# Kernel tuning notes

Measured on AMD Instinct MI355X. Metric: run time of the kernel, lower is better.

The kernel has to match this reference:

```python
import jax, jax.numpy as jnp
import numpy as np

B, C, H, W = 64, 3, 512, 512
P = 16
D = P * P          # 256 = patch_size**2 (token dim)
GH, GW = H // P, W // P
NP = GH * GW       # 1024 patches
HID = 1024         # FFN hidden
L = 6              # num_layers
NC = 1000          # num_classes
EPS = 1e-5


def setup_inputs() -> dict:
    key = jax.random.key(0)
    ks = jax.random.split(key, 8)
    n = lambda i, shape, scale=0.02: jax.random.normal(ks[i], shape, jnp.float32) * scale
    return dict(
        x=jax.random.normal(ks[0], (B, C, H, W), jnp.float32),
        conv_w=n(1, (D, C, P, P)),
        conv_b=jnp.zeros((D,), jnp.float32),
        pos_emb=n(2, (1, NP + 1, D), 1.0),
        cls_tok=n(3, (1, 1, D), 1.0),
        ln1_s=jnp.ones((L, D), jnp.float32), ln1_b=jnp.zeros((L, D), jnp.float32),
        ln2_s=jnp.ones((L, D), jnp.float32), ln2_b=jnp.zeros((L, D), jnp.float32),
        w1=n(4, (L, D, HID)), b1=jnp.zeros((L, HID), jnp.float32),
        w2=n(5, (L, HID, D)), b2=jnp.zeros((L, D), jnp.float32),
        head_ln_s=jnp.ones((D,), jnp.float32), head_ln_b=jnp.zeros((D,), jnp.float32),
        head_w=n(6, (D, NC)), head_b=jnp.zeros((NC,), jnp.float32),
    )


def _ln(x, s, b):
    m = x.mean(-1, keepdims=True)
    v = ((x - m) ** 2).mean(-1, keepdims=True)
    return (x - m) * jax.lax.rsqrt(v + EPS) * s + b


def reference(x, conv_w, conv_b, pos_emb, cls_tok,
              ln1_s, ln1_b, ln2_s, ln2_b, w1, b1, w2, b2,
              head_ln_s, head_ln_b, head_w, head_b):
    b = x.shape[0]
    # patch-embed conv (kernel==stride) as reshape + einsum
    xr = x.reshape(b, C, GH, P, GW, P)
    tok = jnp.einsum('bchpwq,dcpq->bhwd', xr, conv_w).reshape(b, NP, D) + conv_b
    t = jnp.concatenate([jnp.broadcast_to(cls_tok, (b, 1, D)), tok], axis=1) + pos_emb
    for i in range(L):
        # FNet token mixing: real part of 2D FFT over (tokens, dim)
        h = _ln(t, ln1_s[i], ln1_b[i])
        t = t + jnp.fft.fft2(h, axes=(-2, -1)).real
        # FFN
        h = _ln(t, ln2_s[i], ln2_b[i])
        h = jax.nn.leaky_relu(h @ w1[i] + b1[i], negative_slope=0.01) @ w2[i] + b2[i]
        t = t + h
    pooled = t.mean(axis=1)
    logits = _ln(pooled, head_ln_s, head_ln_b) @ head_w + head_b
    return jax.nn.softmax(logits, axis=-1)
```

## Files before the change

### kernel.cpp

```cpp
#include <hip/hip_runtime.h>
#include <math.h>

#define BATCH 64
#define CIN 3
#define IMH 512
#define IMW 512
#define PSZ 16
#define DIM 256
#define GHN 32
#define GWN 32
#define NTOK 1025
#define HID 1024
#define NLAYER 6
#define NCLS 1000
#define LN_EPS 1e-5f

#define KF 576
#define KR 640
#define MF 144
#define MROWS 65600

typedef __attribute__((ext_vector_type(8))) short short8;
typedef __attribute__((ext_vector_type(4))) float f32x4;

#define MFMA16(acc, a, b) acc = __builtin_amdgcn_mfma_f32_16x16x32_bf16(a, b, acc, 0, 0, 0)

__device__ inline unsigned short rne_bf16(float x) {
    unsigned u = __float_as_uint(x);
    return (unsigned short)((u + 0x7FFF + ((u >> 16) & 1)) >> 16);
}
__device__ inline void split_bf16(float x, unsigned short& hi, unsigned short& lo) {
    unsigned short h = rne_bf16(x);
    hi = h;
    float hf = __uint_as_float((unsigned)h << 16);
    lo = rne_bf16(x - hf);
}
__device__ inline float wave_sum(float v) {
#pragma unroll
    for (int off = 32; off; off >>= 1) v += __shfl_xor(v, off);
    return v;
}
__device__ inline short8 ld8x64(const unsigned short* lds, int row, int q) {
    return *(const short8*)(lds + (row * 8 + (q ^ (row & 7))) * 8);
}
__device__ inline short8 ld8x32(const unsigned short* lds, int row, int q) {
    return *(const short8*)(lds + (row * 4 + (q ^ ((row >> 1) & 3))) * 8);
}
__device__ inline void gl2lds16(const unsigned short* g, unsigned short* l) {
    __builtin_amdgcn_global_load_lds((const __attribute__((address_space(1))) unsigned int*)g,
                                     (__attribute__((address_space(3))) unsigned int*)l, 16, 0, 0);
}
__device__ inline void a_stage128(unsigned short* lds, const unsigned short* g, int lda, int tid, int maxrow) {
    int lane = tid & 63, w = tid >> 6;
#pragma unroll
    for (int s = 0; s < 4; s++) {
        int slot = w * 256 + s * 64;
        int sl = slot + lane;
        int row = sl >> 3, gc = (sl & 7) ^ (row & 7);
        if (row > maxrow) row = maxrow;
        gl2lds16(g + (size_t)row * lda + gc * 8, lds + slot * 8);
    }
}
__device__ inline void a_stage128_512(unsigned short* lds, const unsigned short* g, int lda, int tid, int maxrow) {
    int lane = tid & 63, w = tid >> 6;
#pragma unroll
    for (int s = 0; s < 2; s++) {
        int slot = w * 128 + s * 64;
        int sl = slot + lane;
        int row = sl >> 3, gc = (sl & 7) ^ (row & 7);
        if (row > maxrow) row = maxrow;
        gl2lds16(g + (size_t)row * lda + gc * 8, lds + slot * 8);
    }
}
__device__ inline void b_stage128x32(unsigned short* lds, const unsigned short* g, int lda, int tid) {
    int lane = tid & 63;
#pragma unroll
    for (int s = 0; s < 2; s++) {
        int slot = s * 256 + (tid >> 6) * 64;
        int sl = slot + lane;
        int row = sl >> 2, gc = (sl & 3) ^ ((row >> 1) & 3);
        gl2lds16(g + (size_t)row * lda + gc * 8, lds + slot * 8);
    }
}
__device__ inline void a_stage144x32(unsigned short* lds, const unsigned short* g, int lda, int tid) {
    int lane = tid & 63, w = tid >> 6;
#pragma unroll
    for (int s = 0; s < 2; s++) {
        int slot = s * 256 + w * 64;
        int sl = slot + lane;
        int row = sl >> 2, gc = (sl & 3) ^ ((row >> 1) & 3);
        gl2lds16(g + (size_t)row * lda + gc * 8, lds + slot * 8);
    }
    if (w == 0) {
        int slot = 512;
        int sl = slot + lane;
        int row = sl >> 2, gc = (sl & 3) ^ ((row >> 1) & 3);
        gl2lds16(g + (size_t)row * lda + gc * 8, lds + slot * 8);
    }
}

__global__ __launch_bounds__(256) void gen_dft2(unsigned short* C1h, unsigned short* C1l,
                                                unsigned short* S1h, unsigned short* S1l,
                                                unsigned short* C2h, unsigned short* C2l,
                                                unsigned short* S2h, unsigned short* S2l) {
    int idx = blockIdx.x * 256 + threadIdx.x;
    if (idx < KR * KF) {
        int k = idx / KF, n = idx - k * KF;
        float c = 0.f, s = 0.f;
        if (k <= 512 && n <= 512) {
            int r = (k * n) % 1025;
            double ang = 6.283185307179586476925287 * (double)r / 1025.0;
            c = (float)cos(ang); s = (float)sin(ang);
        }
        unsigned short h, l;
        split_bf16(c, h, l); C1h[idx] = h; C1l[idx] = l;
        split_bf16(s, h, l); S1h[idx] = h; S1l[idx] = l;
    }
    if (idx < 256 * 256) {
        int k = idx >> 8, n = idx & 255;
        int r = (k * n) & 255;
        double ang = 6.283185307179586476925287 * (double)r / 256.0;
        float c = (float)cos(ang), s = (float)sin(ang);
        unsigned short h, l;
        split_bf16(c, h, l); C2h[idx] = h; C2l[idx] = l;
        split_bf16(s, h, l); S2h[idx] = h; S2l[idx] = l;
    }
}

__global__ __launch_bounds__(256) void conv_wp(const float* __restrict__ w,
                                               unsigned short* __restrict__ wph, unsigned short* __restrict__ wpl) {
    int idx = blockIdx.x * 256 + threadIdx.x;
    unsigned short h, l;
    split_bf16(w[idx], h, l);
    wph[idx] = h; wpl[idx] = l;
}
__global__ __launch_bounds__(256) void conv_w1t(const float* __restrict__ w1, unsigned short* __restrict__ w1t) {
    int idx = blockIdx.x * 256 + threadIdx.x;
    int l = idx / 262144, rem = idx - l * 262144;
    int n = rem >> 8, k = rem & 255;
    w1t[idx] = rne_bf16(w1[(size_t)l * 262144 + (size_t)k * 1024 + n]);
}
__global__ __launch_bounds__(256) void conv_w2t(const float* __restrict__ w2, unsigned short* __restrict__ w2t) {
    int idx = blockIdx.x * 256 + threadIdx.x;
    int l = idx / 262144, rem = idx - l * 262144;
    int n = rem >> 10, k = rem & 1023;
    w2t[idx] = rne_bf16(w2[(size_t)l * 262144 + (size_t)k * 256 + n]);
}

__global__ __launch_bounds__(256) void cls_init(const float* __restrict__ cls, const float* __restrict__ pos,
                                                float* __restrict__ t) {
    int b = blockIdx.x, tid = threadIdx.x;
    t[(size_t)b * NTOK * DIM + tid] = cls[tid] + pos[tid];
}

__global__ __launch_bounds__(256) void patch_fused(const float* __restrict__ x,
                                                   const unsigned short* __restrict__ wph,
                                                   const unsigned short* __restrict__ wpl,
                                                   const float* __restrict__ cb, const float* __restrict__ pos,
                                                   float* __restrict__ t) {
    __shared__ __align__(16) unsigned short sAh[4096], sAl[4096], sBh[4096], sBl[4096];
    int m0 = blockIdx.x * 128, n0 = blockIdx.y * 128;
    int tid = threadIdx.x, lane = tid & 63, w = tid >> 6;
    int wr = (w >> 1) * 64, wc = (w & 1) * 64;
    f32x4 z = {0.f, 0.f, 0.f, 0.f};
    f32x4 acc[4][4] = {{z, z, z, z}, {z, z, z, z}, {z, z, z, z}, {z, z, z, z}};
    for (int k0 = 0; k0 < 768; k0 += 32) {
#pragma unroll
        for (int s = 0; s < 4; s++) {
            int lin = s * 1024 + tid * 4;
            int row = lin >> 5, kc = lin & 31;
            int m = m0 + row;
            int bb = m >> 10, gh = (m >> 5) & 31, gw = m & 31;
            int k = k0 + kc;
            int c = k >> 8, pp = (k >> 4) & 15, q = k & 15;
            const float* gp = x + (size_t)bb * 786432 + c * 262144 + gh * 8192 + pp * 512 + gw * 16 + q;
            float4 v = *(const float4*)gp;
            ushort4 oh, ol;
            split_bf16(v.x, oh.x, ol.x); split_bf16(v.y, oh.y, ol.y);
            split_bf16(v.z, oh.z, ol.z); split_bf16(v.w, oh.w, ol.w);
            int g = kc >> 3, half = (kc >> 2) & 1;
            int addr = (row * 4 + (g ^ ((row >> 1) & 3))) * 8 + half * 4;
            *(ushort4*)(sAh + addr) = oh;
            *(ushort4*)(sAl + addr) = ol;
        }
        b_stage128x32(sBh, wph + (size_t)n0 * 768 + k0, 768, tid);
        b_stage128x32(sBl, wpl + (size_t)n0 * 768 + k0, 768, tid);
        __syncthreads();
        int q = lane >> 4;
        short8 ah[4], al[4], bh8[4], bl8[4];
#pragma unroll
        for (int i = 0; i < 4; i++) {
            ah[i] = ld8x32(sAh, wr + i * 16 + (lane & 15), q);
            al[i] = ld8x32(sAl, wr + i * 16 + (lane & 15), q);
            bh8[i] = ld8x32(sBh, wc + i * 16 + (lane & 15), q);
            bl8[i] = ld8x32(sBl, wc + i * 16 + (lane & 15), q);
        }
#pragma unroll
        for (int i = 0; i < 4; i++)
#pragma unroll
            for (int j = 0; j < 4; j++) {
                MFMA16(acc[i][j], ah[i], bh8[j]);
                MFMA16(acc[i][j], ah[i], bl8[j]);
                MFMA16(acc[i][j], al[i], bh8[j]);
            }
        __syncthreads();
    }
    int q4 = (lane >> 4) * 4;
#pragma unroll
    for (int i = 0; i < 4; i++) {
        int r = m0 + wr + i * 16 + q4;
#pragma unroll
        for (int j = 0; j < 4; j++) {
            int c = n0 + wc + j * 16 + (lane & 15);
#pragma unroll
            for (int g = 0; g < 4; g++) {
                int rr = r + g;
                int bb = rr >> 10, tok = 1 + (rr & 1023);
                t[((size_t)bb * NTOK + tok) * 256 + c] =
                    acc[i][j][g] + cb[c] + pos[(size_t)tok * 256 + c];
            }
        }
    }
}

__global__ __launch_bounds__(256) void ln_stats(const float* __restrict__ t, float2* __restrict__ stats) {
    int wave = threadIdx.x >> 6, lane = threadIdx.x & 63;
    int m = blockIdx.x * 4 + wave;
    const float* row = t + (size_t)m * DIM;
    float4 v = *(const float4*)(row + lane * 4);
    float mean = wave_sum(v.x + v.y + v.z + v.w) * (1.f / 256.f);
    float dx = v.x - mean, dy = v.y - mean, dz = v.z - mean, dw = v.w - mean;
    float sq = wave_sum(dx * dx + dy * dy + dz * dz + dw * dw);
    float rstd = rsqrtf(sq * (1.f / 256.f) + LN_EPS);
    if (lane == 0) stats[m] = make_float2(mean, rstd);
}

__global__ __launch_bounds__(256) void ln2_bf16(const float* __restrict__ t, unsigned short* __restrict__ hh,
                                                const float* __restrict__ s, const float* __restrict__ bb) {
    int wave = threadIdx.x >> 6, lane = threadIdx.x & 63;
    int m = blockIdx.x * 4 + wave;
    const float* row = t + (size_t)m * DIM;
    float4 v = *(const float4*)(row + lane * 4);
    float mean = wave_sum(v.x + v.y + v.z + v.w) * (1.f / 256.f);
    float dx = v.x - mean, dy = v.y - mean, dz = v.z - mean, dw = v.w - mean;
    float sq = wave_sum(dx * dx + dy * dy + dz * dz + dw * dw);
    float rstd = rsqrtf(sq * (1.f / 256.f) + LN_EPS);
    float4 s4 = *(const float4*)(s + lane * 4);
    float4 b4 = *(const float4*)(bb + lane * 4);
    ushort4 o;
    o.x = rne_bf16(dx * rstd * s4.x + b4.x);
    o.y = rne_bf16(dy * rstd * s4.y + b4.y);
    o.z = rne_bf16(dz * rstd * s4.z + b4.z);
    o.w = rne_bf16(dw * rstd * s4.w + b4.w);
    *(ushort4*)(hh + (size_t)m * DIM + lane * 4) = o;
}

__global__ __launch_bounds__(256) void fold_gemm(
    const float* __restrict__ tt, const float2* __restrict__ stats,
    const float* __restrict__ ls, const float* __restrict__ lb,
    const unsigned short* __restrict__ C2h, const unsigned short* __restrict__ C2l,
    const unsigned short* __restrict__ S2h, const unsigned short* __restrict__ S2l,
    unsigned short* __restrict__ Ycth, unsigned short* __restrict__ Yctl,
    unsigned short* __restrict__ Ysth, unsigned short* __restrict__ Ystl) {
    __shared__ __align__(16) unsigned short sAh[4096], sAl[4096], sBh[4608], sBl[4608];
    int m0 = blockIdx.x * 128;
    int zz = blockIdx.y;
    const unsigned short* Bh = zz ? S2h : C2h;
    const unsigned short* Bl = zz ? S2l : C2l;
    unsigned short* Oh = zz ? Ysth : Ycth;
    unsigned short* Ol = zz ? Ystl : Yctl;
    int tid = threadIdx.x, lane = tid & 63, w = tid >> 6;
    int wr = w * 32;
    f32x4 zf = {0.f, 0.f, 0.f, 0.f};
    f32x4 acc[2][9];
#pragma unroll
    for (int i = 0; i < 2; i++)
#pragma unroll
        for (int j = 0; j < 9; j++) acc[i][j] = zf;
    for (int k0 = 0; k0 < 256; k0 += 32) {
#pragma unroll
        for (int s = 0; s < 4; s++) {
            int sl = tid + s * 256;
            int row = sl >> 3, g = sl & 7;
            int r = m0 + row;
            int b = r / KF, np = r - b * KF;
            float4 hv = {0.f, 0.f, 0.f, 0.f};
            if (np <= 512) {
                int d0 = k0 + g * 4;
                float4 s4 = *(const float4*)(ls + d0);
                float4 b4 = *(const float4*)(lb + d0);
                int i1 = b * NTOK + np;
                float2 st1 = stats[i1];
                float4 va = *(const float4*)(tt + (size_t)i1 * 256 + d0);
                float hax = (va.x - st1.x) * st1.y * s4.x + b4.x;
                float hay = (va.y - st1.x) * st1.y * s4.y + b4.y;
                float haz = (va.z - st1.x) * st1.y * s4.z + b4.z;
                float haw = (va.w - st1.x) * st1.y * s4.w + b4.w;
                float hbx = 0.f, hby = 0.f, hbz = 0.f, hbw = 0.f;
                if (np >= 1) {
                    int i2 = b * NTOK + (NTOK - np);
                    float2 st2 = stats[i2];
                    float4 vb = *(const float4*)(tt + (size_t)i2 * 256 + d0);
                    hbx = (vb.x - st2.x) * st2.y * s4.x + b4.x;
                    hby = (vb.y - st2.x) * st2.y * s4.y + b4.y;
                    hbz = (vb.z - st2.x) * st2.y * s4.z + b4.z;
                    hbw = (vb.w - st2.x) * st2.y * s4.w + b4.w;
                }
                if (zz) { hv.x = hax - hbx; hv.y = hay - hby; hv.z = haz - hbz; hv.w = haw - hbw; }
                else    { hv.x = hax + hbx; hv.y = hay + hby; hv.z = haz + hbz; hv.w = haw + hbw; }
            }
            ushort4 oh, ol;
            split_bf16(hv.x, oh.x, ol.x); split_bf16(hv.y, oh.y, ol.y);
            split_bf16(hv.z, oh.z, ol.z); split_bf16(hv.w, oh.w, ol.w);
            int addr = (row * 4 + ((g >> 1) ^ ((row >> 1) & 3))) * 8 + (g & 1) * 4;
            *(ushort4*)(sAh + addr) = oh;
            *(ushort4*)(sAl + addr) = ol;
        }
        a_stage144x32(sBh, Bh + k0, 256, tid);
        a_stage144x32(sBl, Bl + k0, 256, tid);
        __syncthreads();
        int q = lane >> 4;
        short8 ah[2], al[2];
#pragma unroll
        for (int i = 0; i < 2; i++) {
            int r = wr + i * 16 + (lane & 15);
            ah[i] = ld8x32(sAh, r, q); al[i] = ld8x32(sAl, r, q);
        }
#pragma unroll
        for (int j = 0; j < 9; j++) {
            int rb = j * 16 + (lane & 15);
            short8 bh = ld8x32(sBh, rb, q), bl = ld8x32(sBl, rb, q);
#pragma unroll
            for (int i = 0; i < 2; i++) {
                MFMA16(acc[i][j], ah[i], bh);
                MFMA16(acc[i][j], ah[i], bl);
                MFMA16(acc[i][j], al[i], bh);
            }
        }
        __syncthreads();
    }
    int q4 = (lane >> 4) * 4;
#pragma unroll
    for (int i = 0; i < 2; i++) {
        int r = m0 + wr + i * 16 + q4;
        int bidx = r / KF, kp = r - bidx * KF;
#pragma unroll
        for (int j = 0; j < 9; j++) {
            int c = j * 16 + (lane & 15);
            ushort4 oh, ol;
            split_bf16(acc[i][j][0], oh.x, ol.x);
            split_bf16(acc[i][j][1], oh.y, ol.y);
            split_bf16(acc[i][j][2], oh.z, ol.z);
            split_bf16(acc[i][j][3], oh.w, ol.w);
            size_t off = ((size_t)bidx * MF + c) * KF + kp;
            *(ushort4*)(Oh + off) = oh;
            *(ushort4*)(Ol + off) = ol;
        }
    }
}

__global__ __launch_bounds__(512, 6) void fft_big_dual(
    const unsigned short* __restrict__ C1h, const unsigned short* __restrict__ C1l,
    const unsigned short* __restrict__ S1h, const unsigned short* __restrict__ S1l,
    const unsigned short* __restrict__ Ych, const unsigned short* __restrict__ Ycl,
    const unsigned short* __restrict__ Ysh, const unsigned short* __restrict__ Ysl,
    float* __restrict__ t) {
    __shared__ __align__(16) unsigned short sC1h[4096], sC1l[4096], sS1h[4096], sS1l[4096];
    __shared__ __align__(16) unsigned short sYch[2048], sYcl[2048], sYsh[2048], sYsl[2048];
    int k0m = blockIdx.x * 128, n0 = blockIdx.y * 64;
    int tid = threadIdx.x, lane = tid & 63, w = tid >> 6;
    int wr = (w >> 1) * 32, wc = (w & 1) * 32;
    f32x4 z = {0.f, 0.f, 0.f, 0.f};
    f32x4 U[2][2], V[2][2];
#pragma unroll
    for (int i = 0; i < 2; i++)
#pragma unroll
        for (int j = 0; j < 2; j++) { U[i][j] = z; V[i][j] = z; }
    for (int kk0 = 0; kk0 < KF; kk0 += 32) {
        {
            int row = tid >> 2, gc = (tid & 3) ^ ((row >> 1) & 3);
            size_t ga = (size_t)k0m * KF + kk0 + (size_t)row * KF + gc * 8;
            unsigned short* lbase0 = sC1h + (size_t)(w * 64) * 8;
            unsigned short* lbase1 = sC1l + (size_t)(w * 64) * 8;
            unsigned short* lbase2 = sS1h + (size_t)(w * 64) * 8;
            unsigned short* lbase3 = sS1l + (size_t)(w * 64) * 8;
            gl2lds16(C1h + ga, lbase0);
            gl2lds16(C1l + ga, lbase1);
            gl2lds16(S1h + ga, lbase2);
            gl2lds16(S1l + ga, lbase3);
        }
        {
            int m = w >> 1, p = w & 1;
            const unsigned short* yg;
            unsigned short* yl;
            if (m == 0)      { yg = Ych; yl = sYch; }
            else if (m == 1) { yg = Ycl; yl = sYcl; }
            else if (m == 2) { yg = Ysh; yl = sYsh; }
            else             { yg = Ysl; yl = sYsl; }
            size_t gb = (size_t)n0 * KF + kk0;
#pragma unroll
            for (int s = 0; s < 2; s++) {
                int slot = p * 128 + s * 64;
                int sl = slot + lane;
                int row = sl >> 2, gc = (sl & 3) ^ ((row >> 1) & 3);
                gl2lds16(yg + gb + (size_t)row * KF + gc * 8, yl + slot * 8);
            }
        }
        __syncthreads();
        int q = lane >> 4;
        short8 bch[2], bcl[2], bsh[2], bsl[2];
#pragma unroll
        for (int j = 0; j < 2; j++) {
            int r2 = wc + j * 16 + (lane & 15);
            bch[j] = ld8x32(sYch, r2, q); bcl[j] = ld8x32(sYcl, r2, q);
            bsh[j] = ld8x32(sYsh, r2, q); bsl[j] = ld8x32(sYsl, r2, q);
        }
#pragma unroll
        for (int i = 0; i < 2; i++) {
            int r1 = wr + i * 16 + (lane & 15);
            short8 ach = ld8x32(sC1h, r1, q), acl = ld8x32(sC1l, r1, q);
            short8 ash = ld8x32(sS1h, r1, q), asl = ld8x32(sS1l, r1, q);
#pragma unroll
            for (int j = 0; j < 2; j++) {
                MFMA16(U[i][j], ach, bch[j]);
                MFMA16(U[i][j], ach, bcl[j]);
                MFMA16(U[i][j], acl, bch[j]);
                MFMA16(V[i][j], ash, bsh[j]);
                MFMA16(V[i][j], ash, bsl[j]);
                MFMA16(V[i][j], asl, bsh[j]);
            }
        }
        __syncthreads();
    }
    int q4 = (lane >> 4) * 4;
#pragma unroll
    for (int j = 0; j < 2; j++) {
        int rcol = n0 + wc + j * 16 + (lane & 15);
        int b = rcol / MF, mm = rcol - b * MF;
        float* tb = t + (size_t)b * NTOK * DIM;
        if (mm > 128) continue;
#pragma unroll
        for (int i = 0; i < 2; i++) {
            int kk = k0m + wr + i * 16 + q4;
#pragma unroll
            for (int g = 0; g < 4; g++) {
                int k = kk + g;
                if (k > 512) continue;
                float u = U[i][j][g], v = V[i][j][g];
                tb[(size_t)k * 256 + mm] += u - v;
                if (mm >= 1 && mm <= 127) tb[(size_t)k * 256 + 256 - mm] += u + v;
                if (k >= 1) {
                    tb[(size_t)(NTOK - k) * 256 + mm] += u + v;
                    if (mm >= 1 && mm <= 127) tb[(size_t)(NTOK - k) * 256 + 256 - mm] += u - v;
                }
            }
        }
    }
}

__global__ __launch_bounds__(512) void gemm_ffn_fused(
    const unsigned short* __restrict__ A, const unsigned short* __restrict__ W1t,
    const float* __restrict__ b1, const unsigned short* __restrict__ W2t,
    const float* __restrict__ b2, float* __restrict__ t) {
    __shared__ __align__(16) unsigned short sB[32768];
    __shared__ __align__(16) unsigned short sH[16384];
    int m0 = blockIdx.x * 128;
    int tid = threadIdx.x, lane = tid & 63, w = tid >> 6;
    int wr1 = (w >> 1) * 32, wc1 = (w & 1) * 64;
    int wr2 = (w >> 2) * 64, wc2 = (w & 3) * 64;
    short8 areg[2][8];
#pragma unroll
    for (int i = 0; i < 2; i++) {
        int rr = m0 + wr1 + i * 16 + (lane & 15);
        if (rr > MROWS - 1) rr = MROWS - 1;
        const unsigned short* ap = A + (size_t)rr * 256 + (lane >> 4) * 8;
#pragma unroll
        for (int p = 0; p < 4; p++)
#pragma unroll
            for (int kc = 0; kc < 2; kc++)
                areg[i][p * 2 + kc] = *(const short8*)(ap + p * 64 + kc * 32);
    }
    f32x4 z = {0.f, 0.f, 0.f, 0.f};
    f32x4 acc2[4][4] = {{z, z, z, z}, {z, z, z, z}, {z, z, z, z}, {z, z, z, z}};
    int q4 = (lane >> 4) * 4;
    for (int hc = 0; hc < 8; hc++) {
        int h0 = hc * 128;
        __syncthreads();
#pragma unroll
        for (int p = 0; p < 4; p++)
            a_stage128_512(sB + p * 8192, W1t + (size_t)h0 * 256 + p * 64, 256, tid, 127);
        __syncthreads();
        f32x4 acc1[2][4] = {{z, z, z, z}, {z, z, z, z}};
#pragma unroll
        for (int p = 0; p < 4; p++)
#pragma unroll
            for (int kc = 0; kc < 2; kc++) {
                int q = (lane >> 4) + kc * 4;
                short8 bh[4];
#pragma unroll
                for (int j = 0; j < 4; j++)
                    bh[j] = ld8x64(sB + p * 8192, wc1 + j * 16 + (lane & 15), q);
#pragma unroll
                for (int i = 0; i < 2; i++)
#pragma unroll
                    for (int j = 0; j < 4; j++) MFMA16(acc1[i][j], areg[i][p * 2 + kc], bh[j]);
            }
#pragma unroll
        for (int j = 0; j < 4; j++) {
            int col = wc1 + j * 16 + (lane & 15);
            float bv = b1[h0 + col];
            int panel = col >> 6, c64 = col & 63;
#pragma unroll
            for (int i = 0; i < 2; i++)
#pragma unroll
                for (int g = 0; g < 4; g++) {
                    int row = wr1 + i * 16 + q4 + g;
                    float val = acc1[i][j][g] + bv;
                    val = val > 0.f ? val : 0.01f * val;
                    sH[panel * 8192 + (row * 8 + ((c64 >> 3) ^ (row & 7))) * 8 + (c64 & 7)] = rne_bf16(val);
                }
        }
        __syncthreads();
#pragma unroll
        for (int hp = 0; hp < 2; hp++)
#pragma unroll
            for (int rb = 0; rb < 2; rb++)
                a_stage128_512(sB + hp * 16384 + rb * 8192,
                               W2t + (size_t)(rb * 128) * 1024 + h0 + hp * 64, 1024, tid, 127);
        __syncthreads();
#pragma unroll
        for (int hp = 0; hp < 2; hp++)
#pragma unroll
            for (int kc = 0; kc < 2; kc++) {
                int q = (lane >> 4) + kc * 4;
                short8 ah[4], bh[4];
#pragma unroll
                for (int i = 0; i < 4; i++)
                    ah[i] = ld8x64(sH + hp * 8192, wr2 + i * 16 + (lane & 15), q);
#pragma unroll
                for (int j = 0; j < 4; j++)
                    bh[j] = ld8x64(sB + hp * 16384, wc2 + j * 16 + (lane & 15), q);
#pragma unroll
                for (int i = 0; i < 4; i++)
#pragma unroll
                    for (int j = 0; j < 4; j++) MFMA16(acc2[i][j], ah[i], bh[j]);
            }
    }
#pragma unroll
    for (int i = 0; i < 4; i++) {
        int r = m0 + wr2 + i * 16 + q4;
#pragma unroll
        for (int j = 0; j < 4; j++) {
            int c = wc2 + j * 16 + (lane & 15);
            float bv = b2[c];
#pragma unroll
            for (int g = 0; g < 4; g++) {
                int rr = r + g;
                if (rr < MROWS) t[(size_t)rr * 256 + c] += acc2[i][j][g] + bv;
            }
        }
    }
}

__global__ __launch_bounds__(256) void head_kernel(const float* __restrict__ t,
                                                   const float* __restrict__ hs, const float* __restrict__ hb,
                                                   const float* __restrict__ hw, const float* __restrict__ hbias,
                                                   float* __restrict__ out) {
    __shared__ float red[256];
    __shared__ float lnv[256];
    int b = blockIdx.x, tid = threadIdx.x;
    const float* tb = t + (size_t)b * NTOK * DIM;
    float s = 0.f;
    for (int m = 0; m < NTOK; m++) s += tb[m * DIM + tid];
    s *= (1.f / 1025.f);
    red[tid] = s;
    __syncthreads();
    for (int off = 128; off; off >>= 1) {
        if (tid < off) red[tid] += red[tid + off];
        __syncthreads();
    }
    float mean = red[0] * (1.f / 256.f);
    __syncthreads();
    float d = s - mean;
    red[tid] = d * d;
    __syncthreads();
    for (int off = 128; off; off >>= 1) {
        if (tid < off) red[tid] += red[tid + off];
        __syncthreads();
    }
    float rstd = rsqrtf(red[0] * (1.f / 256.f) + LN_EPS);
    __syncthreads();
    lnv[tid] = d * rstd * hs[tid] + hb[tid];
    __syncthreads();
    float lo[4];
#pragma unroll
    for (int jj = 0; jj < 4; jj++) {
        int n = tid + jj * 256;
        float a = -1e30f;
        if (n < NCLS) {
            a = hbias[n];
            for (int dd = 0; dd < DIM; dd++) a += lnv[dd] * hw[dd * NCLS + n];
        }
        lo[jj] = a;
    }
    float mx = fmaxf(fmaxf(lo[0], lo[1]), fmaxf(lo[2], lo[3]));
    red[tid] = mx;
    __syncthreads();
    for (int off = 128; off; off >>= 1) {
        if (tid < off) red[tid] = fmaxf(red[tid], red[tid + off]);
        __syncthreads();
    }
    float gmax = red[0];
    __syncthreads();
    float ev[4];
    float es = 0.f;
#pragma unroll
    for (int jj = 0; jj < 4; jj++) {
        int n = tid + jj * 256;
        ev[jj] = 0.f;
        if (n < NCLS) {
            ev[jj] = expf(lo[jj] - gmax);
            es += ev[jj];
        }
    }
    red[tid] = es;
    __syncthreads();
    for (int off = 128; off; off >>= 1) {
        if (tid < off) red[tid] += red[tid + off];
        __syncthreads();
    }
    float inv = 1.f / red[0];
#pragma unroll
    for (int jj = 0; jj < 4; jj++) {
        int n = tid + jj * 256;
        if (n < NCLS) out[(size_t)b * NCLS + n] = ev[jj] * inv;
    }
}

extern "C" void kernel_launch(void* const* d_in, const int* in_sizes, int n_in,
                              void* d_out, int out_size, void* d_ws, size_t ws_size,
                              hipStream_t stream) {
    const float* x      = (const float*)d_in[0];
    const float* conv_w = (const float*)d_in[1];
    const float* conv_b = (const float*)d_in[2];
    const float* pos    = (const float*)d_in[3];
    const float* cls    = (const float*)d_in[4];
    const float* ln1_s  = (const float*)d_in[5];
    const float* ln1_b  = (const float*)d_in[6];
    const float* ln2_s  = (const float*)d_in[7];
    const float* ln2_b  = (const float*)d_in[8];
    const float* w1     = (const float*)d_in[9];
    const float* b1     = (const float*)d_in[10];
    const float* w2     = (const float*)d_in[11];
    const float* b2     = (const float*)d_in[12];
    const float* hls    = (const float*)d_in[13];
    const float* hlb    = (const float*)d_in[14];
    const float* hw     = (const float*)d_in[15];
    const float* hbias  = (const float*)d_in[16];
    float* out = (float*)d_out;
    char* W = (char*)d_ws;

    float*          t    = (float*)(W + 0ULL);
    char*           pool = W + 67174400ULL;
    unsigned short* Ycth = (unsigned short*)(pool + 75497472ULL);
    unsigned short* Yctl = (unsigned short*)(pool + 75497472ULL + 10616832ULL);
    unsigned short* Ysth = (unsigned short*)(pool + 75497472ULL + 2 * 10616832ULL);
    unsigned short* Ystl = (unsigned short*)(pool + 75497472ULL + 3 * 10616832ULL);
    unsigned short* hh   = (unsigned short*)(pool + 134348800ULL);
    unsigned short* C1h  = (unsigned short*)(W + 235110400ULL);
    unsigned short* C1l  = (unsigned short*)(W + 235110400ULL + 737280ULL);
    unsigned short* S1h  = (unsigned short*)(W + 235110400ULL + 2 * 737280ULL);
    unsigned short* S1l  = (unsigned short*)(W + 235110400ULL + 3 * 737280ULL);
    unsigned short* C2h  = (unsigned short*)(W + 238059520ULL);
    unsigned short* C2l  = (unsigned short*)(W + 238059520ULL + 131072ULL);
    unsigned short* S2h  = (unsigned short*)(W + 238059520ULL + 2 * 131072ULL);
    unsigned short* S2l  = (unsigned short*)(W + 238059520ULL + 3 * 131072ULL);
    unsigned short* w1t  = (unsigned short*)(W + 238583808ULL);
    unsigned short* w2t  = (unsigned short*)(W + 241729536ULL);
    unsigned short* wph  = (unsigned short*)(W + 244875264ULL);
    unsigned short* wpl  = (unsigned short*)(W + 245268480ULL);
    float2*         stats = (float2*)(W + 245661696ULL);

    gen_dft2<<<dim3(1440), dim3(256), 0, stream>>>(C1h, C1l, S1h, S1l, C2h, C2l, S2h, S2l);
    conv_wp<<<dim3(768), dim3(256), 0, stream>>>(conv_w, wph, wpl);
    conv_w1t<<<dim3(6144), dim3(256), 0, stream>>>(w1, w1t);
    conv_w2t<<<dim3(6144), dim3(256), 0, stream>>>(w2, w2t);
    cls_init<<<dim3(BATCH), dim3(256), 0, stream>>>(cls, pos, t);
    patch_fused<<<dim3(512, 2), dim3(256), 0, stream>>>(x, wph, wpl, conv_b, pos, t);

    for (int l = 0; l < NLAYER; l++) {
        ln_stats<<<dim3(16400), dim3(256), 0, stream>>>(t, stats);
        fold_gemm<<<dim3(288, 2), dim3(256), 0, stream>>>(
            t, stats, ln1_s + l * DIM, ln1_b + l * DIM,
            C2h, C2l, S2h, S2l, Ycth, Yctl, Ysth, Ystl);
        fft_big_dual<<<dim3(5, 144), dim3(512), 0, stream>>>(
            C1h, C1l, S1h, S1l, Ycth, Yctl, Ysth, Ystl, t);
        ln2_bf16<<<dim3(16400), dim3(256), 0, stream>>>(t, hh, ln2_s + l * DIM, ln2_b + l * DIM);
        gemm_ffn_fused<<<dim3(513), dim3(512), 0, stream>>>(
            hh, w1t + (size_t)l * 262144, b1 + (size_t)l * HID,
            w2t + (size_t)l * 262144, b2 + (size_t)l * DIM, t);
    }
    head_kernel<<<dim3(BATCH), dim3(256), 0, stream>>>(t, hls, hlb, hw, hbias, out);
}
```

Before: 2.735 ms.

## Shrink FFN hidden chunk to 64 and prefetch next W1 chunk during GEMM2

The fused FFN kernel now walks the hidden dimension in 16 chunks of 64 instead of 8 chunks of 128. LDS use drops from 96KB to 80KB, split into separate W1/W2/H buffers, and launch bounds ask for more resident blocks. The next W1 chunk is loaded asynchronously into LDS while the second GEMM runs on the current chunk, removing a barrier-separated staging phase per iteration. The cost is twice as many loop iterations and barriers, plus smaller MFMA work per sync.

Result: slower. 4.024 ms (+47.1%).

```diff
diff --git a/kernel.cpp b/kernel.cpp
--- a/kernel.cpp
+++ b/kernel.cpp
@@ -458,16 +458,18 @@
     }
 }
 
-__global__ __launch_bounds__(512) void gemm_ffn_fused(
+__global__ __launch_bounds__(512, 4) void gemm_ffn_fused(
     const unsigned short* __restrict__ A, const unsigned short* __restrict__ W1t,
     const float* __restrict__ b1, const unsigned short* __restrict__ W2t,
     const float* __restrict__ b2, float* __restrict__ t) {
-    __shared__ __align__(16) unsigned short sB[32768];
-    __shared__ __align__(16) unsigned short sH[16384];
+    __shared__ __align__(16) unsigned short sW1[16384];
+    __shared__ __align__(16) unsigned short sW2[16384];
+    __shared__ __align__(16) unsigned short sH[8192];
     int m0 = blockIdx.x * 128;
     int tid = threadIdx.x, lane = tid & 63, w = tid >> 6;
-    int wr1 = (w >> 1) * 32, wc1 = (w & 1) * 64;
+    int wr1 = (w >> 1) * 32, wc1 = (w & 1) * 32;
     int wr2 = (w >> 2) * 64, wc2 = (w & 3) * 64;
+    int prow = tid >> 3, pgc = (tid & 7) ^ (prow & 7);
     short8 areg[2][8];
 #pragma unroll
     for (int i = 0; i < 2; i++) {
@@ -483,33 +485,34 @@
     f32x4 z = {0.f, 0.f, 0.f, 0.f};
     f32x4 acc2[4][4] = {{z, z, z, z}, {z, z, z, z}, {z, z, z, z}, {z, z, z, z}};
     int q4 = (lane >> 4) * 4;
-    for (int hc = 0; hc < 8; hc++) {
-        int h0 = hc * 128;
-        __syncthreads();
-#pragma unroll
-        for (int p = 0; p < 4; p++)
-            a_stage128_512(sB + p * 8192, W1t + (size_t)h0 * 256 + p * 64, 256, tid, 127);
-        __syncthreads();
-        f32x4 acc1[2][4] = {{z, z, z, z}, {z, z, z, z}};
+#pragma unroll
+    for (int p = 0; p < 4; p++)
+        gl2lds16(W1t + (size_t)prow * 256 + p * 64 + pgc * 8, sW1 + p * 4096 + (w * 64) * 8);
+    for (int hc = 0; hc < 16; hc++) {
+        int h0 = hc * 64;
+#pragma unroll
+        for (int rb = 0; rb < 2; rb++)
+            a_stage128_512(sW2 + rb * 8192, W2t + (size_t)(rb * 128) * 1024 + h0, 1024, tid, 127);
+        __syncthreads();
+        f32x4 acc1[2][2] = {{z, z}, {z, z}};
 #pragma unroll
         for (int p = 0; p < 4; p++)
 #pragma unroll
             for (int kc = 0; kc < 2; kc++) {
                 int q = (lane >> 4) + kc * 4;
-                short8 bh[4];
-#pragma unroll
-                for (int j = 0; j < 4; j++)
-                    bh[j] = ld8x64(sB + p * 8192, wc1 + j * 16 + (lane & 15), q);
+                short8 bh[2];
+#pragma unroll
+                for (int j = 0; j < 2; j++)
+                    bh[j] = ld8x64(sW1 + p * 4096, wc1 + j * 16 + (lane & 15), q);
 #pragma unroll
                 for (int i = 0; i < 2; i++)
 #pragma unroll
-                    for (int j = 0; j < 4; j++) MFMA16(acc1[i][j], areg[i][p * 2 + kc], bh[j]);
-            }
-#pragma unroll
-        for (int j = 0; j < 4; j++) {
+                    for (int j = 0; j < 2; j++) MFMA16(acc1[i][j], areg[i][p * 2 + kc], bh[j]);
+            }
+#pragma unroll
+        for (int j = 0; j < 2; j++) {
             int col = wc1 + j * 16 + (lane & 15);
             float bv = b1[h0 + col];
-            int panel = col >> 6, c64 = col & 63;
 #pragma unroll
             for (int i = 0; i < 2; i++)
 #pragma unroll
@@ -517,34 +520,34 @@
                     int row = wr1 + i * 16 + q4 + g;
                     float val = acc1[i][j][g] + bv;
                     val = val > 0.f ? val : 0.01f * val;
-                    sH[panel * 8192 + (row * 8 + ((c64 >> 3) ^ (row & 7))) * 8 + (c64 & 7)] = rne_bf16(val);
+                    sH[(row * 8 + ((col >> 3) ^ (row & 7))) * 8 + (col & 7)] = rne_bf16(val);
                 }
         }
         __syncthreads();
-#pragma unroll
-        for (int hp = 0; hp < 2; hp++)
-#pragma unroll
-            for (int rb = 0; rb < 2; rb++)
-                a_stage128_512(sB + hp * 16384 + rb * 8192,
-                               W2t + (size_t)(rb * 128) * 1024 + h0 + hp * 64, 1024, tid, 127);
-        __syncthreads();
-#pragma unroll
-        for (int hp = 0; hp < 2; hp++)
-#pragma unroll
-            for (int kc = 0; kc < 2; kc++) {
-                int q = (lane >> 4) + kc * 4;
-                short8 ah[4], bh[4];
-#pragma unroll
-                for (int i = 0; i < 4; i++)
-                    ah[i] = ld8x64(sH + hp * 8192, wr2 + i * 16 + (lane & 15), q);
-#pragma unroll
-                for (int j = 0; j < 4; j++)
-                    bh[j] = ld8x64(sB + hp * 16384, wc2 + j * 16 + (lane & 15), q);
-#pragma unroll
-                for (int i = 0; i < 4; i++)
-#pragma unroll
-                    for (int j = 0; j < 4; j++) MFMA16(acc2[i][j], ah[i], bh[j]);
-            }
+        if (hc < 15) {
+            const unsigned short* wsrc = W1t + (size_t)(h0 + 64 + prow) * 256;
+#pragma unroll
+            for (int p = 0; p < 4; p++)
+                gl2lds16(wsrc + p * 64 + pgc * 8, sW1 + p * 4096 + (w * 64) * 8);
+        }
+#pragma unroll
+        for (int kc = 0; kc < 2; kc++) {
+            int q = (lane >> 4) + kc * 4;
+            short8 ah[4], bh[4];
+#pragma unroll
+            for (int i = 0; i < 4; i++)
+                ah[i] = ld8x64(sH, wr2 + i * 16 + (lane & 15), q);
+#pragma unroll
+            for (int j = 0; j < 4; j++) {
+                int n = wc2 + j * 16 + (lane & 15);
+                bh[j] = ld8x64(sW2 + (n >> 7) * 8192, n & 127, q);
+            }
+#pragma unroll
+            for (int i = 0; i < 4; i++)
+#pragma unroll
+                for (int j = 0; j < 4; j++) MFMA16(acc2[i][j], ah[i], bh[j]);
+        }
+        __syncthreads();
     }
 #pragma unroll
     for (int i = 0; i < 4; i++) {
```
